# Kernel optimization log

Hardware: AMD Instinct MI355X
Metric: run time of the kernel (lower is better)

Reference implementation:

```python
import jax, jax.numpy as jnp
import numpy as np

IMAGE_SIZE = 256
SIGMA = 1.0   # soft-rasterization sharpness (pixels)
EPS = 1e-8


def _quat_to_rot(q):
    q = q / jnp.sqrt(jnp.sum(q * q) + EPS)
    w, x, y, z = q[0], q[1], q[2], q[3]
    return jnp.stack([
        jnp.stack([1 - 2 * (y * y + z * z), 2 * (x * y - w * z), 2 * (x * z + w * y)]),
        jnp.stack([2 * (x * y + w * z), 1 - 2 * (x * x + z * z), 2 * (y * z - w * x)]),
        jnp.stack([2 * (x * z - w * y), 2 * (y * z + w * x), 1 - 2 * (x * x + y * y)]),
    ])


def _render_silhouette(vertices, faces, q, t, K):
    # camera transform: v_cam = R(q) v + t   [V,3]
    R = _quat_to_rot(q)
    vc = vertices[0] @ R.T + t
    z = vc[:, 2] + EPS
    # perspective projection to pixel coords
    px_v = K[0, 0] * vc[:, 0] / z + K[0, 2]
    py_v = K[1, 1] * vc[:, 1] / z + K[1, 2]
    verts2d = jnp.stack([px_v, py_v], axis=-1)          # [V,2]
    tri = verts2d[faces[0]]                             # [F,3,2]

    e01 = tri[:, 1] - tri[:, 0]
    e02 = tri[:, 2] - tri[:, 0]
    area2 = e01[:, 0] * e02[:, 1] - e01[:, 1] * e02[:, 0]
    s = jnp.where(area2 >= 0, 1.0, -1.0)                # [F]

    # pixel centers
    ii, jj = jnp.meshgrid(jnp.arange(IMAGE_SIZE), jnp.arange(IMAGE_SIZE), indexing='ij')
    px = (jj.astype(jnp.float32) + 0.5).reshape(-1)     # [P]
    py = (ii.astype(jnp.float32) + 0.5).reshape(-1)     # [P]

    # signed distance to triangle = min over edges of normalized edge function
    d = None
    for k in range(3):
        a = tri[:, k]
        b = tri[:, (k + 1) % 3]
        ex = b[:, 0] - a[:, 0]
        ey = b[:, 1] - a[:, 1]
        inv_len = s / jnp.sqrt(ex * ex + ey * ey + EPS)  # sign folded in
        cx = -ey * inv_len
        cy = ex * inv_len
        c0 = (ey * a[:, 0] - ex * a[:, 1]) * inv_len
        c = px[:, None] * cx[None, :] + py[:, None] * cy[None, :] + c0[None, :]  # [P,F]
        d = c if d is None else jnp.minimum(d, c)

    # soft coverage: alpha = 1 - prod_F (1 - sigmoid(d/sigma))
    log_not_cov = jax.nn.log_sigmoid(-d / SIGMA)         # [P,F]
    sil = 1.0 - jnp.exp(jnp.sum(log_not_cov, axis=1))    # [P]
    return sil.reshape(IMAGE_SIZE, IMAGE_SIZE)


def setup_inputs() -> dict:
    key = jax.random.key(0)
    k1, k2, k3 = jax.random.split(key, 3)
    V, F = 1000, 1000
    vertices = jax.random.normal(k1, (1, V, 3), jnp.float32) * 0.3
    faces = jax.random.randint(k2, (1, F, 3), 0, V, jnp.int32)
    image_ref = jax.random.uniform(k3, (IMAGE_SIZE, IMAGE_SIZE), dtype=jnp.float32)
    q = jnp.array([1.0, 0.05, -0.03, 0.02], dtype=jnp.float32)
    t = jnp.array([0.0, 0.0, 2.732], dtype=jnp.float32)
    K = jnp.array([[280.0, 0.0, 128.0], [0.0, 280.0, 128.0], [0.0, 0.0, 1.0]], dtype=jnp.float32)
    return {"vertices": vertices, "faces": faces, "q": q, "t": t, "K": K, "image_ref": image_ref}


def reference(vertices, faces, q, t, K, image_ref):
    image = _render_silhouette(vertices, faces, q, t, K)   # [256,256]
    loss = jnp.mean((image - image_ref) ** 2, axis=1)      # per-row mean, [256]
    return loss
```

## Files before the change

kernel.cpp:

```cpp
#include <hip/hip_runtime.h>
#include <math.h>

#define IMG 256
#define NFACE 1000
#define NFP 1024
#define NWAVE 4
#define CAP 1024
#define EPSF 1e-8f
#define LOG2E 1.44269504088896f
#define TCUT 16.0f
#define ACC_BREAK 25.0f
#define RSLACK 7.15f

__device__ float g_soa[9][NFP];

__global__ __launch_bounds__(256) void k_coeff(const float* __restrict__ verts,
                                               const int* __restrict__ faces,
                                               const float* __restrict__ q,
                                               const float* __restrict__ t,
                                               const float* __restrict__ K,
                                               float* __restrict__ out) {
    int f = blockIdx.x * 256 + threadIdx.x;
    if (blockIdx.x == 0 && threadIdx.x < IMG) out[threadIdx.x] = 0.f;
    if (f >= NFP) return;

    float c[9];
    if (f < NFACE) {
        float qw = q[0], qx = q[1], qy = q[2], qz = q[3];
        float qn = sqrtf(qw * qw + qx * qx + qy * qy + qz * qz + EPSF);
        qw /= qn; qx /= qn; qy /= qn; qz /= qn;
        float R00 = 1.f - 2.f * (qy * qy + qz * qz);
        float R01 = 2.f * (qx * qy - qw * qz);
        float R02 = 2.f * (qx * qz + qw * qy);
        float R10 = 2.f * (qx * qy + qw * qz);
        float R11 = 1.f - 2.f * (qx * qx + qz * qz);
        float R12 = 2.f * (qy * qz - qw * qx);
        float R20 = 2.f * (qx * qz - qw * qy);
        float R21 = 2.f * (qy * qz + qw * qx);
        float R22 = 1.f - 2.f * (qx * qx + qy * qy);
        float tx = t[0], ty = t[1], tz = t[2];
        float K00 = K[0], K02 = K[2], K11 = K[4], K12 = K[5];

        float X[3], Y[3];
#pragma unroll
        for (int k = 0; k < 3; ++k) {
            int vi = faces[f * 3 + k];
            float vx = verts[vi * 3 + 0];
            float vy = verts[vi * 3 + 1];
            float vz = verts[vi * 3 + 2];
            float cx = R00 * vx + R01 * vy + R02 * vz + tx;
            float cy = R10 * vx + R11 * vy + R12 * vz + ty;
            float cz = R20 * vx + R21 * vy + R22 * vz + tz;
            float z = cz + EPSF;
            X[k] = K00 * cx / z + K02;
            Y[k] = K11 * cy / z + K12;
        }

        float e01x = X[1] - X[0], e01y = Y[1] - Y[0];
        float e02x = X[2] - X[0], e02y = Y[2] - Y[0];
        float area2 = e01x * e02y - e01y * e02x;
        float s = (area2 >= 0.f) ? LOG2E : -LOG2E;

#pragma unroll
        for (int k = 0; k < 3; ++k) {
            int k1 = (k + 1) % 3;
            float ex = X[k1] - X[k];
            float ey = Y[k1] - Y[k];
            float inv = s / sqrtf(ex * ex + ey * ey + EPSF);
            c[k * 3 + 0] = -ey * inv;
            c[k * 3 + 1] = ex * inv;
            c[k * 3 + 2] = (ey * X[k] - ex * Y[k]) * inv;
        }
    } else {
        c[0] = 0.f; c[1] = 0.f; c[2] = -1e9f;
        c[3] = 0.f; c[4] = 0.f; c[5] = -1e9f;
        c[6] = 0.f; c[7] = 0.f; c[8] = -1e9f;
    }

#pragma unroll
    for (int k = 0; k < 9; ++k) g_soa[k][f] = c[k];
}

__global__ __launch_bounds__(256) void k_main(const float* __restrict__ image_ref,
                                              float* __restrict__ out) {
    const int tid = threadIdx.x;
    const int wave = tid >> 6;
    const int lane = tid & 63;
    const int x0 = blockIdx.x * 8, y0 = blockIdx.y * 8;
    const float tcx = x0 + 4.0f;
    const float tcy = y0 + 4.0f;

    __shared__ float4 s_cf[CAP * 3];
    __shared__ float s_acc[NWAVE][64];
    __shared__ float s_S[NWAVE];
    __shared__ int s_cnt;

    if (tid == 0) s_cnt = 0;
    __syncthreads();

    const int wbase = wave * 256;
    float slb = 0.f;
    for (int r = 0; r < 4; ++r) {
        const int f = wbase + r * 64 + lane;
        float l0 = g_soa[0][f], l1 = g_soa[1][f], l2 = g_soa[2][f];
        float l3 = g_soa[3][f], l4 = g_soa[4][f], l5 = g_soa[5][f];
        float l6 = g_soa[6][f], l7 = g_soa[7][f], l8 = g_soa[8][f];
        float c0 = fmaf(tcx, l0, fmaf(tcy, l1, l2));
        float c1 = fmaf(tcx, l3, fmaf(tcy, l4, l5));
        float c2 = fmaf(tcx, l6, fmaf(tcy, l7, l8));
        float mc = fminf(fminf(c0, c1), c2);
        slb += fmaxf(mc - RSLACK, 0.f);
        float e0 = c0 + 3.5f * (fabsf(l0) + fabsf(l1));
        float e1 = c1 + 3.5f * (fabsf(l3) + fabsf(l4));
        float e2 = c2 + 3.5f * (fabsf(l6) + fabsf(l7));
        bool hit = (fminf(fminf(e0, e1), e2) > -TCUT);
        unsigned long long msk = __ballot(hit);
        int n = __popcll(msk);
        int base = 0;
        if (lane == 0) base = atomicAdd(&s_cnt, n);
        base = __builtin_amdgcn_readfirstlane(base);
        int pos = base + __popcll(msk & ((1ull << lane) - 1ull));
        if (hit) {
            s_cf[pos * 3 + 0] = make_float4(l0, l1, l2, 0.f);
            s_cf[pos * 3 + 1] = make_float4(l3, l4, l5, 0.f);
            s_cf[pos * 3 + 2] = make_float4(l6, l7, l8, 0.f);
        }
    }
#pragma unroll
    for (int o = 1; o < 64; o <<= 1) slb += __shfl_xor(slb, o);
    if (lane == 0) s_S[wave] = slb;
    __syncthreads();

    const int cnt = s_cnt;
    const int cntp = (cnt + 31) & ~31;
    if (tid < cntp - cnt) {
        int ppos = cnt + tid;
        s_cf[ppos * 3 + 0] = make_float4(0.f, 0.f, -1e9f, 0.f);
        s_cf[ppos * 3 + 1] = make_float4(0.f, 0.f, -1e9f, 0.f);
        s_cf[ppos * 3 + 2] = make_float4(0.f, 0.f, -1e9f, 0.f);
    }
    __syncthreads();
    const float S_tile = s_S[0] + s_S[1] + s_S[2] + s_S[3];

    if (S_tile <= ACC_BREAK) {
        const int fs = lane >> 3;
        const int ii = lane & 7;
        const float pxc = x0 + ii + 0.5f;
        float acc[8], p[8];
#pragma unroll
        for (int g = 0; g < 8; ++g) { acc[g] = 0.f; p[g] = 1.f; }

        const int nj = cntp >> 3;
        for (int j = wave; j < nj; j += 4) {
            const int base = (j * 8 + fs) * 3;
            float4 A = s_cf[base + 0];
            float4 B = s_cf[base + 1];
            float4 C = s_cf[base + 2];
#pragma unroll
            for (int g = 0; g < 8; ++g) {
                float pyc = y0 + g + 0.5f;
                float u = fminf(fminf(fmaf(pxc, A.x, fmaf(pyc, A.y, A.z)),
                                      fmaf(pxc, B.x, fmaf(pyc, B.y, B.z))),
                                fmaf(pxc, C.x, fmaf(pyc, C.y, C.z)));
                acc[g] += fmaxf(u, 0.f);
                float e = __builtin_amdgcn_exp2f(-fabsf(u));
                p[g] = fmaf(p[g], e, p[g]);
            }
        }
#pragma unroll
        for (int g = 0; g < 8; ++g) {
            float a = acc[g] + __builtin_amdgcn_logf(p[g]);
            a += __shfl_xor(a, 8);
            a += __shfl_xor(a, 16);
            a += __shfl_xor(a, 32);
            if (fs == g) s_acc[wave][g * 8 + ii] = a;
        }
    }
    __syncthreads();

    if (wave == 0) {
        const int col = x0 + (lane & 7);
        const int row = y0 + (lane >> 3);
        float tot = (S_tile > ACC_BREAK)
                        ? 32.f
                        : (s_acc[0][lane] + s_acc[1][lane] +
                           s_acc[2][lane] + s_acc[3][lane]);
        float sil = 1.f - __builtin_amdgcn_exp2f(-tot);
        float d = sil - image_ref[row * IMG + col];
        float v = d * d;
        v += __shfl_xor(v, 1);
        v += __shfl_xor(v, 2);
        v += __shfl_xor(v, 4);
        if ((lane & 7) == 0) atomicAdd(&out[row], v * (1.f / 256.f));
    }
}

extern "C" void kernel_launch(void* const* d_in, const int* in_sizes, int n_in,
                              void* d_out, int out_size, void* d_ws, size_t ws_size,
                              hipStream_t stream) {
    const float* verts = (const float*)d_in[0];
    const int* faces = (const int*)d_in[1];
    const float* q = (const float*)d_in[2];
    const float* t = (const float*)d_in[3];
    const float* K = (const float*)d_in[4];
    const float* image_ref = (const float*)d_in[5];
    float* out = (float*)d_out;

    k_coeff<<<NFP / 256, 256, 0, stream>>>(verts, faces, q, t, K, out);
    k_main<<<dim3(IMG / 8, IMG / 8), 256, 0, stream>>>(image_ref, out);
}
```

Baseline: 20.63 us.

## Fuse coefficient kernel into main kernel and use last-block row reduction

Removes the separate per-face coefficient kernel: every tile block now recomputes the projected edge coefficients for all 1000 faces directly from vertices and faces before culling. It also replaces per-row float atomics on the output with per-block partials written to a global buffer, where the last block of each row band (found with a counter) does a deterministic reduction and resets the counter. This saves a kernel launch and the output zeroing, at the cost of 1024-fold redundant projection work (gathers, divides, sqrts) and a threadfence plus a global counter handshake.

```diff
diff --git a/kernel.cpp b/kernel.cpp
--- a/kernel.cpp
+++ b/kernel.cpp
@@ -12,81 +12,21 @@
 #define ACC_BREAK 25.0f
 #define RSLACK 7.15f
 
-__device__ float g_soa[9][NFP];
-
-__global__ __launch_bounds__(256) void k_coeff(const float* __restrict__ verts,
-                                               const int* __restrict__ faces,
-                                               const float* __restrict__ q,
-                                               const float* __restrict__ t,
-                                               const float* __restrict__ K,
-                                               float* __restrict__ out) {
-    int f = blockIdx.x * 256 + threadIdx.x;
-    if (blockIdx.x == 0 && threadIdx.x < IMG) out[threadIdx.x] = 0.f;
-    if (f >= NFP) return;
-
-    float c[9];
-    if (f < NFACE) {
-        float qw = q[0], qx = q[1], qy = q[2], qz = q[3];
-        float qn = sqrtf(qw * qw + qx * qx + qy * qy + qz * qz + EPSF);
-        qw /= qn; qx /= qn; qy /= qn; qz /= qn;
-        float R00 = 1.f - 2.f * (qy * qy + qz * qz);
-        float R01 = 2.f * (qx * qy - qw * qz);
-        float R02 = 2.f * (qx * qz + qw * qy);
-        float R10 = 2.f * (qx * qy + qw * qz);
-        float R11 = 1.f - 2.f * (qx * qx + qz * qz);
-        float R12 = 2.f * (qy * qz - qw * qx);
-        float R20 = 2.f * (qx * qz - qw * qy);
-        float R21 = 2.f * (qy * qz + qw * qx);
-        float R22 = 1.f - 2.f * (qx * qx + qy * qy);
-        float tx = t[0], ty = t[1], tz = t[2];
-        float K00 = K[0], K02 = K[2], K11 = K[4], K12 = K[5];
-
-        float X[3], Y[3];
-#pragma unroll
-        for (int k = 0; k < 3; ++k) {
-            int vi = faces[f * 3 + k];
-            float vx = verts[vi * 3 + 0];
-            float vy = verts[vi * 3 + 1];
-            float vz = verts[vi * 3 + 2];
-            float cx = R00 * vx + R01 * vy + R02 * vz + tx;
-            float cy = R10 * vx + R11 * vy + R12 * vz + ty;
-            float cz = R20 * vx + R21 * vy + R22 * vz + tz;
-            float z = cz + EPSF;
-            X[k] = K00 * cx / z + K02;
-            Y[k] = K11 * cy / z + K12;
-        }
-
-        float e01x = X[1] - X[0], e01y = Y[1] - Y[0];
-        float e02x = X[2] - X[0], e02y = Y[2] - Y[0];
-        float area2 = e01x * e02y - e01y * e02x;
-        float s = (area2 >= 0.f) ? LOG2E : -LOG2E;
-
-#pragma unroll
-        for (int k = 0; k < 3; ++k) {
-            int k1 = (k + 1) % 3;
-            float ex = X[k1] - X[k];
-            float ey = Y[k1] - Y[k];
-            float inv = s / sqrtf(ex * ex + ey * ey + EPSF);
-            c[k * 3 + 0] = -ey * inv;
-            c[k * 3 + 1] = ex * inv;
-            c[k * 3 + 2] = (ey * X[k] - ex * Y[k]) * inv;
-        }
-    } else {
-        c[0] = 0.f; c[1] = 0.f; c[2] = -1e9f;
-        c[3] = 0.f; c[4] = 0.f; c[5] = -1e9f;
-        c[6] = 0.f; c[7] = 0.f; c[8] = -1e9f;
-    }
-
-#pragma unroll
-    for (int k = 0; k < 9; ++k) g_soa[k][f] = c[k];
-}
-
-__global__ __launch_bounds__(256) void k_main(const float* __restrict__ image_ref,
-                                              float* __restrict__ out) {
+__device__ float g_rp[IMG][32];
+__device__ int g_bc[32];
+
+__global__ __launch_bounds__(256) void k_all(const float* __restrict__ verts,
+                                             const int* __restrict__ faces,
+                                             const float* __restrict__ q,
+                                             const float* __restrict__ t,
+                                             const float* __restrict__ K,
+                                             const float* __restrict__ image_ref,
+                                             float* __restrict__ out) {
     const int tid = threadIdx.x;
     const int wave = tid >> 6;
     const int lane = tid & 63;
-    const int x0 = blockIdx.x * 8, y0 = blockIdx.y * 8;
+    const int bx = blockIdx.x, by = blockIdx.y;
+    const int x0 = bx * 8, y0 = by * 8;
     const float tcx = x0 + 4.0f;
     const float tcy = y0 + 4.0f;
 
@@ -94,25 +34,74 @@
     __shared__ float s_acc[NWAVE][64];
     __shared__ float s_S[NWAVE];
     __shared__ int s_cnt;
+    __shared__ int s_last;
 
     if (tid == 0) s_cnt = 0;
     __syncthreads();
+
+    float qw = q[0], qx = q[1], qy = q[2], qz = q[3];
+    float qn = sqrtf(qw * qw + qx * qx + qy * qy + qz * qz + EPSF);
+    qw /= qn; qx /= qn; qy /= qn; qz /= qn;
+    const float R00 = 1.f - 2.f * (qy * qy + qz * qz);
+    const float R01 = 2.f * (qx * qy - qw * qz);
+    const float R02 = 2.f * (qx * qz + qw * qy);
+    const float R10 = 2.f * (qx * qy + qw * qz);
+    const float R11 = 1.f - 2.f * (qx * qx + qz * qz);
+    const float R12 = 2.f * (qy * qz - qw * qx);
+    const float R20 = 2.f * (qx * qz - qw * qy);
+    const float R21 = 2.f * (qy * qz + qw * qx);
+    const float R22 = 1.f - 2.f * (qx * qx + qy * qy);
+    const float tx = t[0], ty = t[1], tz = t[2];
+    const float K00 = K[0], K02 = K[2], K11 = K[4], K12 = K[5];
 
     const int wbase = wave * 256;
     float slb = 0.f;
     for (int r = 0; r < 4; ++r) {
         const int f = wbase + r * 64 + lane;
-        float l0 = g_soa[0][f], l1 = g_soa[1][f], l2 = g_soa[2][f];
-        float l3 = g_soa[3][f], l4 = g_soa[4][f], l5 = g_soa[5][f];
-        float l6 = g_soa[6][f], l7 = g_soa[7][f], l8 = g_soa[8][f];
-        float c0 = fmaf(tcx, l0, fmaf(tcy, l1, l2));
-        float c1 = fmaf(tcx, l3, fmaf(tcy, l4, l5));
-        float c2 = fmaf(tcx, l6, fmaf(tcy, l7, l8));
+        float c[9];
+        if (f < NFACE) {
+            float X[3], Y[3];
+#pragma unroll
+            for (int k = 0; k < 3; ++k) {
+                int vi = faces[f * 3 + k];
+                float vx = verts[vi * 3 + 0];
+                float vy = verts[vi * 3 + 1];
+                float vz = verts[vi * 3 + 2];
+                float cx = R00 * vx + R01 * vy + R02 * vz + tx;
+                float cy = R10 * vx + R11 * vy + R12 * vz + ty;
+                float cz = R20 * vx + R21 * vy + R22 * vz + tz;
+                float z = cz + EPSF;
+                X[k] = K00 * cx / z + K02;
+                Y[k] = K11 * cy / z + K12;
+            }
+            float e01x = X[1] - X[0], e01y = Y[1] - Y[0];
+            float e02x = X[2] - X[0], e02y = Y[2] - Y[0];
+            float area2 = e01x * e02y - e01y * e02x;
+            float s = (area2 >= 0.f) ? LOG2E : -LOG2E;
+#pragma unroll
+            for (int k = 0; k < 3; ++k) {
+                int k1 = (k + 1) % 3;
+                float ex = X[k1] - X[k];
+                float ey = Y[k1] - Y[k];
+                float inv = s / sqrtf(ex * ex + ey * ey + EPSF);
+                c[k * 3 + 0] = -ey * inv;
+                c[k * 3 + 1] = ex * inv;
+                c[k * 3 + 2] = (ey * X[k] - ex * Y[k]) * inv;
+            }
+        } else {
+            c[0] = 0.f; c[1] = 0.f; c[2] = -1e9f;
+            c[3] = 0.f; c[4] = 0.f; c[5] = -1e9f;
+            c[6] = 0.f; c[7] = 0.f; c[8] = -1e9f;
+        }
+
+        float c0 = fmaf(tcx, c[0], fmaf(tcy, c[1], c[2]));
+        float c1 = fmaf(tcx, c[3], fmaf(tcy, c[4], c[5]));
+        float c2 = fmaf(tcx, c[6], fmaf(tcy, c[7], c[8]));
         float mc = fminf(fminf(c0, c1), c2);
         slb += fmaxf(mc - RSLACK, 0.f);
-        float e0 = c0 + 3.5f * (fabsf(l0) + fabsf(l1));
-        float e1 = c1 + 3.5f * (fabsf(l3) + fabsf(l4));
-        float e2 = c2 + 3.5f * (fabsf(l6) + fabsf(l7));
+        float e0 = c0 + 3.5f * (fabsf(c[0]) + fabsf(c[1]));
+        float e1 = c1 + 3.5f * (fabsf(c[3]) + fabsf(c[4]));
+        float e2 = c2 + 3.5f * (fabsf(c[6]) + fabsf(c[7]));
         bool hit = (fminf(fminf(e0, e1), e2) > -TCUT);
         unsigned long long msk = __ballot(hit);
         int n = __popcll(msk);
@@ -121,9 +110,9 @@
         base = __builtin_amdgcn_readfirstlane(base);
         int pos = base + __popcll(msk & ((1ull << lane) - 1ull));
         if (hit) {
-            s_cf[pos * 3 + 0] = make_float4(l0, l1, l2, 0.f);
-            s_cf[pos * 3 + 1] = make_float4(l3, l4, l5, 0.f);
-            s_cf[pos * 3 + 2] = make_float4(l6, l7, l8, 0.f);
+            s_cf[pos * 3 + 0] = make_float4(c[0], c[1], c[2], 0.f);
+            s_cf[pos * 3 + 1] = make_float4(c[3], c[4], c[5], 0.f);
+            s_cf[pos * 3 + 2] = make_float4(c[6], c[7], c[8], 0.f);
         }
     }
 #pragma unroll
@@ -191,7 +180,22 @@
         v += __shfl_xor(v, 1);
         v += __shfl_xor(v, 2);
         v += __shfl_xor(v, 4);
-        if ((lane & 7) == 0) atomicAdd(&out[row], v * (1.f / 256.f));
+        if ((lane & 7) == 0) g_rp[row][bx] = v;
+        __threadfence();
+        if (lane == 0) {
+            int old = atomicAdd(&g_bc[by], 1);
+            s_last = (old == 31);
+        }
+    }
+    __syncthreads();
+
+    if (s_last) {
+        __threadfence();
+        float v = g_rp[y0 + (tid >> 5)][tid & 31] * (1.f / 256.f);
+#pragma unroll
+        for (int o = 1; o < 32; o <<= 1) v += __shfl_xor(v, o);
+        if ((tid & 31) == 0) out[y0 + (tid >> 5)] = v;
+        if (tid == 0) g_bc[by] = 0;
     }
 }
 
@@ -206,6 +210,5 @@
     const float* image_ref = (const float*)d_in[5];
     float* out = (float*)d_out;
 
-    k_coeff<<<NFP / 256, 256, 0, stream>>>(verts, faces, q, t, K, out);
-    k_main<<<dim3(IMG / 8, IMG / 8), 256, 0, stream>>>(image_ref, out);
+    k_all<<<dim3(32, 32), 256, 0, stream>>>(verts, faces, q, t, K, image_ref, out);
 }
```

Measured after the change: 44.48 us. 116% more time.

## Replace per-tile face compaction with full global face loop and empty-tile skip

Applied to the files above, without the earlier changes.

The per-tile compaction of candidate faces into shared memory (ballot, atomic counter, scatter, padding) is removed. Each tile now only records whether any face is near it and skips the tile when none is. Tiles that have a near face loop over all 1024 faces, reading AoS float4 coefficients from global memory that k_coeff also writes. This cuts shared-memory traffic and syncs, but tiles with any nearby face now evaluate every face instead of only the culled subset.

```diff
diff --git a/kernel.cpp b/kernel.cpp
--- a/kernel.cpp
+++ b/kernel.cpp
@@ -5,7 +5,6 @@
 #define NFACE 1000
 #define NFP 1024
 #define NWAVE 4
-#define CAP 1024
 #define EPSF 1e-8f
 #define LOG2E 1.44269504088896f
 #define TCUT 16.0f
@@ -13,6 +12,7 @@
 #define RSLACK 7.15f
 
 __device__ float g_soa[9][NFP];
+__device__ float4 g_cf[NFP * 3];
 
 __global__ __launch_bounds__(256) void k_coeff(const float* __restrict__ verts,
                                                const int* __restrict__ faces,
@@ -79,6 +79,9 @@
 
 #pragma unroll
     for (int k = 0; k < 9; ++k) g_soa[k][f] = c[k];
+    g_cf[f * 3 + 0] = make_float4(c[0], c[1], c[2], 0.f);
+    g_cf[f * 3 + 1] = make_float4(c[3], c[4], c[5], 0.f);
+    g_cf[f * 3 + 2] = make_float4(c[6], c[7], c[8], 0.f);
 }
 
 __global__ __launch_bounds__(256) void k_main(const float* __restrict__ image_ref,
@@ -90,16 +93,14 @@
     const float tcx = x0 + 4.0f;
     const float tcy = y0 + 4.0f;
 
-    __shared__ float4 s_cf[CAP * 3];
     __shared__ float s_acc[NWAVE][64];
     __shared__ float s_S[NWAVE];
-    __shared__ int s_cnt;
-
-    if (tid == 0) s_cnt = 0;
-    __syncthreads();
+    __shared__ int s_any[NWAVE];
 
     const int wbase = wave * 256;
     float slb = 0.f;
+    bool anyhit = false;
+#pragma unroll
     for (int r = 0; r < 4; ++r) {
         const int f = wbase + r * 64 + lane;
         float l0 = g_soa[0][f], l1 = g_soa[1][f], l2 = g_soa[2][f];
@@ -113,36 +114,20 @@
         float e0 = c0 + 3.5f * (fabsf(l0) + fabsf(l1));
         float e1 = c1 + 3.5f * (fabsf(l3) + fabsf(l4));
         float e2 = c2 + 3.5f * (fabsf(l6) + fabsf(l7));
-        bool hit = (fminf(fminf(e0, e1), e2) > -TCUT);
-        unsigned long long msk = __ballot(hit);
-        int n = __popcll(msk);
-        int base = 0;
-        if (lane == 0) base = atomicAdd(&s_cnt, n);
-        base = __builtin_amdgcn_readfirstlane(base);
-        int pos = base + __popcll(msk & ((1ull << lane) - 1ull));
-        if (hit) {
-            s_cf[pos * 3 + 0] = make_float4(l0, l1, l2, 0.f);
-            s_cf[pos * 3 + 1] = make_float4(l3, l4, l5, 0.f);
-            s_cf[pos * 3 + 2] = make_float4(l6, l7, l8, 0.f);
-        }
+        anyhit = anyhit || (fminf(fminf(e0, e1), e2) > -TCUT);
     }
 #pragma unroll
     for (int o = 1; o < 64; o <<= 1) slb += __shfl_xor(slb, o);
-    if (lane == 0) s_S[wave] = slb;
-    __syncthreads();
-
-    const int cnt = s_cnt;
-    const int cntp = (cnt + 31) & ~31;
-    if (tid < cntp - cnt) {
-        int ppos = cnt + tid;
-        s_cf[ppos * 3 + 0] = make_float4(0.f, 0.f, -1e9f, 0.f);
-        s_cf[ppos * 3 + 1] = make_float4(0.f, 0.f, -1e9f, 0.f);
-        s_cf[ppos * 3 + 2] = make_float4(0.f, 0.f, -1e9f, 0.f);
+    const int anyw = __any(anyhit) ? 1 : 0;
+    if (lane == 0) {
+        s_S[wave] = slb;
+        s_any[wave] = anyw;
     }
     __syncthreads();
     const float S_tile = s_S[0] + s_S[1] + s_S[2] + s_S[3];
+    const int band = (s_any[0] | s_any[1] | s_any[2] | s_any[3]);
 
-    if (S_tile <= ACC_BREAK) {
+    if (S_tile <= ACC_BREAK && band) {
         const int fs = lane >> 3;
         const int ii = lane & 7;
         const float pxc = x0 + ii + 0.5f;
@@ -150,12 +135,11 @@
 #pragma unroll
         for (int g = 0; g < 8; ++g) { acc[g] = 0.f; p[g] = 1.f; }
 
-        const int nj = cntp >> 3;
-        for (int j = wave; j < nj; j += 4) {
+        for (int j = wave; j < NFP / 8; j += 4) {
             const int base = (j * 8 + fs) * 3;
-            float4 A = s_cf[base + 0];
-            float4 B = s_cf[base + 1];
-            float4 C = s_cf[base + 2];
+            float4 A = g_cf[base + 0];
+            float4 B = g_cf[base + 1];
+            float4 C = g_cf[base + 2];
 #pragma unroll
             for (int g = 0; g < 8; ++g) {
                 float pyc = y0 + g + 0.5f;
@@ -181,10 +165,11 @@
     if (wave == 0) {
         const int col = x0 + (lane & 7);
         const int row = y0 + (lane >> 3);
-        float tot = (S_tile > ACC_BREAK)
-                        ? 32.f
-                        : (s_acc[0][lane] + s_acc[1][lane] +
-                           s_acc[2][lane] + s_acc[3][lane]);
+        float tot;
+        if (S_tile > ACC_BREAK) tot = 32.f;
+        else if (!band) tot = 0.f;
+        else tot = s_acc[0][lane] + s_acc[1][lane] +
+                   s_acc[2][lane] + s_acc[3][lane];
         float sil = 1.f - __builtin_amdgcn_exp2f(-tot);
         float d = sil - image_ref[row * IMG + col];
         float v = d * d;
```

After: 37.07 us. 1.8x slower.
